# Performance work log

Hardware: AMD Instinct MI355X
Metric: run time of the kernel (lower is better)

Reference implementation:

```python
import jax, jax.numpy as jnp
import numpy as np

HIDDEN = 512
NUM_HEADS = 8
HEAD = HIDDEN // NUM_HEADS
TOP_K = 64
NEG = -1e9


def setup_inputs() -> dict:
    key = jax.random.key(0)
    ks = jax.random.split(key, 12)
    B, Q, S = 2, 2048, 4096
    sc = 0.02
    return {
        "main_input": jax.random.normal(ks[0], (B, Q, HIDDEN), jnp.float32),
        "side_input": jax.random.normal(ks[1], (S, HIDDEN), jnp.float32),
        "att_mask": jax.random.randint(ks[2], (B, Q, S), 0, 2, jnp.int32),
        "Wq": jax.random.normal(ks[3], (HIDDEN, HIDDEN), jnp.float32) * sc,
        "bq": jnp.zeros((HIDDEN,), jnp.float32),
        "Wk": jax.random.normal(ks[4], (HIDDEN, HIDDEN), jnp.float32) * sc,
        "bk": jnp.zeros((HIDDEN,), jnp.float32),
        "Wv": jax.random.normal(ks[5], (HIDDEN, HIDDEN), jnp.float32) * sc,
        "bv": jnp.zeros((HIDDEN,), jnp.float32),
        "Wo": jax.random.normal(ks[6], (HIDDEN, HIDDEN), jnp.float32) * sc,
        "bo": jnp.zeros((HIDDEN,), jnp.float32),
    }


def reference(main_input, side_input, att_mask, Wq, bq, Wk, bk, Wv, bv, Wo, bo):
    B, Qlen, _ = main_input.shape
    S = side_input.shape[0]
    # multi-head projections; side K/V shared across the whole batch
    q = (main_input @ Wq + bq).reshape(B, Qlen, NUM_HEADS, HEAD)
    k = (side_input @ Wk + bk).reshape(S, NUM_HEADS, HEAD)
    v = (side_input @ Wv + bv).reshape(S, NUM_HEADS, HEAD)
    # scores: [B, H, Q, S]
    scores = jnp.einsum("bqhd,khd->bhqk", q, k) / jnp.sqrt(jnp.asarray(HEAD, q.dtype))
    # attention mask (0 = masked)
    mask = att_mask[:, None, :, :].astype(scores.dtype)  # [B,1,Q,S]
    scores = scores + (1.0 - mask) * NEG
    # top-k restriction: keep only the TOP_K largest scores per query row
    thresh = jax.lax.top_k(scores, TOP_K)[0][..., -1:]  # kth largest
    scores = jnp.where(scores >= thresh, scores, NEG)
    probs = jax.nn.softmax(scores, axis=-1)
    ctx = jnp.einsum("bhqk,khd->bqhd", probs, v).reshape(B, Qlen, HIDDEN)
    return ctx @ Wo + bo
```

## Files before the change

### kernel.cpp

```cpp
#include <hip/hip_runtime.h>
#include <stdint.h>

typedef uint32_t u32;
typedef unsigned long long u64;

#define NEGV (-1e9f)
#define MAXSEL 128
#define NCAND 12

__device__ __forceinline__ u32 f2ord(float f) {
  u32 x = __float_as_uint(f);
  return (x & 0x80000000u) ? ~x : (x | 0x80000000u);
}
__device__ __forceinline__ float ord2f(u32 u) {
  u32 x = (u & 0x80000000u) ? (u ^ 0x80000000u) : ~u;
  return __uint_as_float(x);
}

__global__ __launch_bounds__(256)
void pack_mask(const int* __restrict__ mask, u64* __restrict__ mbits) {
  int w = blockIdx.x * 256 + threadIdx.x;
  const int4* p = (const int4*)(mask + (size_t)w * 64);
  u64 bits = 0;
#pragma unroll
  for (int j = 0; j < 16; ++j) {
    int4 m = p[j];
    if (m.x) bits |= 1ull << (j * 4 + 0);
    if (m.y) bits |= 1ull << (j * 4 + 1);
    if (m.z) bits |= 1ull << (j * 4 + 2);
    if (m.w) bits |= 1ull << (j * 4 + 3);
  }
  mbits[w] = bits;
}

__global__ __launch_bounds__(256)
void gemm_bias(const float* __restrict__ A, const float* __restrict__ W,
               const float* __restrict__ bias, float* __restrict__ C) {
  __shared__ float As[16][68];
  __shared__ float Bs[16][64];
  const int tid = threadIdx.x;
  const int tx = tid & 15, ty = tid >> 4;
  const int n0 = blockIdx.x << 6, m0 = blockIdx.y << 6;
  float c[4][4] = {};
  for (int k0 = 0; k0 < 512; k0 += 16) {
    {
      const int row = tid >> 2, kp = (tid & 3) << 2;
      float4 av = *(const float4*)&A[(size_t)(m0 + row) * 512 + k0 + kp];
      As[kp + 0][row] = av.x;
      As[kp + 1][row] = av.y;
      As[kp + 2][row] = av.z;
      As[kp + 3][row] = av.w;
      const int kk = tid >> 4, np = (tid & 15) << 2;
      *(float4*)&Bs[kk][np] = *(const float4*)&W[(size_t)(k0 + kk) * 512 + n0 + np];
    }
    __syncthreads();
#pragma unroll
    for (int kk = 0; kk < 16; ++kk) {
      float4 a = *(const float4*)&As[kk][ty << 2];
      float4 b = *(const float4*)&Bs[kk][tx << 2];
      c[0][0] += a.x * b.x; c[0][1] += a.x * b.y; c[0][2] += a.x * b.z; c[0][3] += a.x * b.w;
      c[1][0] += a.y * b.x; c[1][1] += a.y * b.y; c[1][2] += a.y * b.z; c[1][3] += a.y * b.w;
      c[2][0] += a.z * b.x; c[2][1] += a.z * b.y; c[2][2] += a.z * b.z; c[2][3] += a.z * b.w;
      c[3][0] += a.w * b.x; c[3][1] += a.w * b.y; c[3][2] += a.w * b.z; c[3][3] += a.w * b.w;
    }
    __syncthreads();
  }
  float4 bv = *(const float4*)&bias[n0 + (tx << 2)];
#pragma unroll
  for (int i = 0; i < 4; ++i) {
    float4 o;
    o.x = c[i][0] + bv.x; o.y = c[i][1] + bv.y;
    o.z = c[i][2] + bv.z; o.w = c[i][3] + bv.w;
    *(float4*)&C[(size_t)(m0 + (ty << 2) + i) * 512 + n0 + (tx << 2)] = o;
  }
}

__global__ __launch_bounds__(256)
void gemm_bias_T(const float* __restrict__ A, const float* __restrict__ W,
                 const float* __restrict__ bias, float* __restrict__ CT, int qsh) {
  __shared__ float As[16][68];
  __shared__ float Bs[16][64];
  const int tid = threadIdx.x;
  const int tx = tid & 15, ty = tid >> 4;
  const int n0 = blockIdx.x << 6, m0 = blockIdx.y << 6;
  float c[4][4] = {};
  for (int k0 = 0; k0 < 512; k0 += 16) {
    {
      const int row = tid >> 2, kp = (tid & 3) << 2;
      float4 av = *(const float4*)&A[(size_t)(m0 + row) * 512 + k0 + kp];
      As[kp + 0][row] = av.x;
      As[kp + 1][row] = av.y;
      As[kp + 2][row] = av.z;
      As[kp + 3][row] = av.w;
      const int kk = tid >> 4, np = (tid & 15) << 2;
      *(float4*)&Bs[kk][np] = *(const float4*)&W[(size_t)(k0 + kk) * 512 + n0 + np];
    }
    __syncthreads();
#pragma unroll
    for (int kk = 0; kk < 16; ++kk) {
      float4 a = *(const float4*)&As[kk][ty << 2];
      float4 b = *(const float4*)&Bs[kk][tx << 2];
      c[0][0] += a.x * b.x; c[0][1] += a.x * b.y; c[0][2] += a.x * b.z; c[0][3] += a.x * b.w;
      c[1][0] += a.y * b.x; c[1][1] += a.y * b.y; c[1][2] += a.y * b.z; c[1][3] += a.y * b.w;
      c[2][0] += a.z * b.x; c[2][1] += a.z * b.y; c[2][2] += a.z * b.z; c[2][3] += a.z * b.w;
      c[3][0] += a.w * b.x; c[3][1] += a.w * b.y; c[3][2] += a.w * b.z; c[3][3] += a.w * b.w;
    }
    __syncthreads();
  }
  float4 bv = *(const float4*)&bias[n0 + (tx << 2)];
  float bvv[4] = {bv.x, bv.y, bv.z, bv.w};
  const int qlen = 1 << qsh;
  const int qmask = qlen - 1;
#pragma unroll
  for (int i = 0; i < 4; ++i) {
#pragma unroll
    for (int j = 0; j < 4; ++j) {
      float val = c[i][j] + bvv[j];
      int m = m0 + (ty << 2) + i;
      int n = n0 + (tx << 2) + j;
      int h = n >> 6, d = n & 63;
      int bb = m >> qsh, q = m & qmask;
      CT[(((size_t)bb * 8 + h) * 64 + d) * qlen + q] = val;
    }
  }
}

__global__ __launch_bounds__(256)
void score_kernel(const float* __restrict__ qT, const float* __restrict__ kT,
                  const u64* __restrict__ mbits, float* __restrict__ sbuf, int sl0) {
  __shared__ float Qs[64][128];
  __shared__ float Ks[64][128];
  const int sl = sl0 + blockIdx.z;
  const int b = sl >> 3, h = sl & 7;
  const int s0 = blockIdx.x << 7, q0 = blockIdx.y << 7;
  const int tid = threadIdx.x;
  const float* qbase = qT + (size_t)sl * 64 * 2048 + q0;
  const float* kbase = kT + (size_t)h * 64 * 4096 + s0;
  float4* Qf = (float4*)&Qs[0][0];
  float4* Kf = (float4*)&Ks[0][0];
#pragma unroll
  for (int u = 0; u < 8; ++u) {
    int i = (u << 8) + tid;
    int row = i >> 5, col = (i & 31) << 2;
    Qf[i] = *(const float4*)(qbase + (size_t)row * 2048 + col);
    Kf[i] = *(const float4*)(kbase + (size_t)row * 4096 + col);
  }
  __syncthreads();
  const int tx = tid & 15, ty = tid >> 4;
  float c[8][8] = {};
#pragma unroll 4
  for (int g = 0; g < 16; ++g) {
    const int kk = g << 2;
    float qa[8][4], kb[8][4];
#pragma unroll
    for (int t = 0; t < 4; ++t) {
#pragma unroll
      for (int i = 0; i < 8; ++i) qa[i][t] = Qs[kk + t][(ty << 3) + i];
#pragma unroll
      for (int j = 0; j < 4; ++j) {
        kb[j][t]     = Ks[kk + t][(tx << 2) + j];
        kb[4 + j][t] = Ks[kk + t][64 + (tx << 2) + j];
      }
    }
#pragma unroll
    for (int i = 0; i < 8; ++i)
#pragma unroll
      for (int j = 0; j < 8; ++j)
        c[i][j] += qa[i][0] * kb[j][0] + qa[i][1] * kb[j][1]
                 + qa[i][2] * kb[j][2] + qa[i][3] * kb[j][3];
  }
  float* srow = sbuf + ((size_t)blockIdx.z * 2048 + q0) * 4096 + s0;
  const u64* mrow = mbits + ((size_t)(b * 2048 + q0)) * 64 + (s0 >> 6);
#pragma unroll
  for (int i = 0; i < 8; ++i) {
    const int row = (ty << 3) + i;
    u64 wA = mrow[(size_t)row * 64];
    u64 wB = mrow[(size_t)row * 64 + 1];
    float4 o0, o1;
    o0.x = ((wA >> ((tx << 2) + 0)) & 1) ? c[i][0] * 0.125f : NEGV;
    o0.y = ((wA >> ((tx << 2) + 1)) & 1) ? c[i][1] * 0.125f : NEGV;
    o0.z = ((wA >> ((tx << 2) + 2)) & 1) ? c[i][2] * 0.125f : NEGV;
    o0.w = ((wA >> ((tx << 2) + 3)) & 1) ? c[i][3] * 0.125f : NEGV;
    o1.x = ((wB >> ((tx << 2) + 0)) & 1) ? c[i][4] * 0.125f : NEGV;
    o1.y = ((wB >> ((tx << 2) + 1)) & 1) ? c[i][5] * 0.125f : NEGV;
    o1.z = ((wB >> ((tx << 2) + 2)) & 1) ? c[i][6] * 0.125f : NEGV;
    o1.w = ((wB >> ((tx << 2) + 3)) & 1) ? c[i][7] * 0.125f : NEGV;
    *(float4*)&srow[(size_t)row * 4096 + (tx << 2)] = o0;
    *(float4*)&srow[(size_t)row * 4096 + 64 + (tx << 2)] = o1;
  }
}

__global__ __launch_bounds__(256)
void select_kernel(const float* __restrict__ sbuf, const float* __restrict__ vbuf,
                   float* __restrict__ ctxbuf, int sl0) {
  const int sl = sl0 + blockIdx.y;
  const int b = sl >> 3, h = sl & 7;
  const int w = threadIdx.x >> 6, lane = threadIdx.x & 63;
  const int qi = (blockIdx.x << 2) + w;
  __shared__ u32  cv_lds[4][NCAND][64];
  __shared__ int  ci_lds[4][NCAND][64];
  __shared__ int   s_idx[4][MAXSEL];
  __shared__ float s_e[4][MAXSEL];

  const float* srow = sbuf + ((size_t)blockIdx.y * 2048 + qi) * 4096;
  const u32 ordneg = f2ord(NEGV);
  const u64 lmask_lt = (1ull << lane) - 1ull;

  u32 u[64];
#pragma unroll
  for (int j = 0; j < 16; ++j) {
    float4 v = *(const float4*)(srow + (j << 8) + (lane << 2));
    u[j * 4 + 0] = f2ord(v.x);
    u[j * 4 + 1] = f2ord(v.y);
    u[j * 4 + 2] = f2ord(v.z);
    u[j * 4 + 3] = f2ord(v.w);
  }
  u32 lmax = 0;
#pragma unroll
  for (int e = 0; e < 64; ++e) lmax = u[e] > lmax ? u[e] : lmax;
  u32 mx = lmax, mn = lmax;
#pragma unroll
  for (int off = 32; off; off >>= 1) {
    u32 a = (u32)__shfl_xor((int)mx, off, 64);
    u32 bq = (u32)__shfl_xor((int)mn, off, 64);
    mx = a > mx ? a : mx;
    mn = bq < mn ? bq : mn;
  }
  const float fm = ord2f(mx);
  const u32 lo0 = mn;

  int cnt = 0;
#pragma unroll
  for (int e = 0; e < 64; ++e) {
    u32 ue = u[e];
    if (ue >= lo0 && ue != ordneg) {
      if (cnt < NCAND) {
        cv_lds[w][cnt][lane] = ue;
        ci_lds[w][cnt][lane] = ((e >> 2) << 8) + (lane << 2) + (e & 3);
      }
      cnt++;
    }
  }
  const bool fallback = (__ballot(cnt > NCAND) != 0ull);

  u32 thr;
  int nsel;
  float esum = 0.f;

  if (!fallback) {
    asm volatile("s_waitcnt lgkmcnt(0)" ::: "memory");
    u32 cv[NCAND];
    int ci[NCAND];
#pragma unroll
    for (int j = 0; j < NCAND; ++j) {
      u32 raw = cv_lds[w][j][lane];
      cv[j] = (j < cnt) ? raw : 0u;
      ci[j] = ci_lds[w][j][lane];
    }
    u32 lo = lo0, hi = mx + 1;
    while (hi - lo > 1) {
      u32 mid = lo + ((hi - lo) >> 1);
      int c2 = 0;
#pragma unroll
      for (int j = 0; j < NCAND; ++j)
        c2 += __popcll(__ballot(cv[j] >= mid));
      if (c2 >= 64) lo = mid; else hi = mid;
    }
    thr = lo;
    int base = 0;
#pragma unroll
    for (int j = 0; j < NCAND; ++j) {
      bool pred = (j < cnt) && (cv[j] >= thr);
      u64 m = __ballot(pred);
      int ofs = base + __popcll(m & lmask_lt);
      if (pred && ofs < MAXSEL) {
        float ev = __expf(ord2f(cv[j]) - fm);
        s_idx[w][ofs] = ci[j];
        s_e[w][ofs] = ev;
        esum += ev;
      }
      base += (int)__popcll(m);
    }
    nsel = base < MAXSEL ? base : MAXSEL;
  } else {
    u32 lo = ordneg, hi = mx + 1;
    while (hi - lo > 1) {
      u32 mid = lo + ((hi - lo) >> 1);
      int c2 = 0;
#pragma unroll
      for (int e = 0; e < 64; ++e)
        c2 += __popcll(__ballot(u[e] >= mid));
      if (c2 >= 64) lo = mid; else hi = mid;
    }
    thr = lo;
    int base = 0;
#pragma unroll
    for (int e = 0; e < 64; ++e) {
      bool pred = (u[e] >= thr) && (u[e] != ordneg);
      u64 m = __ballot(pred);
      int ofs = base + __popcll(m & lmask_lt);
      if (pred && ofs < MAXSEL) {
        float ev = __expf(ord2f(u[e]) - fm);
        s_idx[w][ofs] = ((e >> 2) << 8) + (lane << 2) + (e & 3);
        s_e[w][ofs] = ev;
        esum += ev;
      }
      base += (int)__popcll(m);
    }
    nsel = base < MAXSEL ? base : MAXSEL;
  }

#pragma unroll
  for (int off = 32; off; off >>= 1) esum += __shfl_xor(esum, off, 64);
  const float rs = 1.0f / esum;
  asm volatile("s_waitcnt lgkmcnt(0)" ::: "memory");

  float acc = 0.f;
  const float* vb = vbuf + h * 64 + lane;
#pragma unroll 4
  for (int j = 0; j < nsel; ++j)
    acc += s_e[w][j] * vb[(size_t)s_idx[w][j] << 9];
  ctxbuf[((size_t)(b * 2048 + qi)) * 512 + h * 64 + lane] = acc * rs;
}

extern "C" void kernel_launch(void* const* d_in, const int* in_sizes, int n_in,
                              void* d_out, int out_size, void* d_ws, size_t ws_size,
                              hipStream_t stream) {
  const float* main_in = (const float*)d_in[0];
  const float* side_in = (const float*)d_in[1];
  const int*   mask    = (const int*)d_in[2];
  const float* Wq = (const float*)d_in[3];
  const float* bq = (const float*)d_in[4];
  const float* Wk = (const float*)d_in[5];
  const float* bk = (const float*)d_in[6];
  const float* Wv = (const float*)d_in[7];
  const float* bv = (const float*)d_in[8];
  const float* Wo = (const float*)d_in[9];
  const float* bo = (const float*)d_in[10];
  float* out = (float*)d_out;

  char* ws = (char*)d_ws;
  float* qT   = (float*)(ws);
  float* kT   = (float*)(ws + ((size_t)8 << 20));
  float* vbuf = (float*)(ws + ((size_t)16 << 20));
  float* ctxb = (float*)(ws + ((size_t)24 << 20));
  u64* mbits  = (u64*)(ws + ((size_t)32 << 20));
  float* sbuf = (float*)(ws + ((size_t)34 << 20));
  const size_t base = (size_t)34 << 20;
  const size_t sliceb = (size_t)2048 * 4096 * 4;

  int nz = 1;
  if (ws_size > base + sliceb) {
    size_t m = (ws_size - base) / sliceb;
    nz = (int)(m > 16 ? 16 : m);
  }

  pack_mask<<<1024, 256, 0, stream>>>(mask, mbits);
  gemm_bias_T<<<dim3(8, 64), 256, 0, stream>>>(main_in, Wq, bq, qT, 11);
  gemm_bias_T<<<dim3(8, 64), 256, 0, stream>>>(side_in, Wk, bk, kT, 12);
  gemm_bias  <<<dim3(8, 64), 256, 0, stream>>>(side_in, Wv, bv, vbuf);

  for (int sl0 = 0; sl0 < 16; sl0 += nz) {
    int z = nz < (16 - sl0) ? nz : (16 - sl0);
    score_kernel <<<dim3(32, 16, z), 256, 0, stream>>>(qT, kT, mbits, sbuf, sl0);
    select_kernel<<<dim3(512, z), 256, 0, stream>>>(sbuf, vbuf, ctxb, sl0);
  }

  gemm_bias<<<dim3(8, 64), 256, 0, stream>>>(ctxb, Wo, bo, out);
}
```

Measured before the change: 824.6 us.

## Restructure top-k select kernel to one wave per block with unified selection pass

The select kernel now runs one 64-lane wave per block (2048 blocks instead of 512 blocks of four waves), with launch bounds of (64, 2). The candidate count rises from 12 to 16. The index LDS array is dropped: after the threshold search, a single shared pass over all 64 register values builds a packed (index, exp) list in shared memory. The gather over V is unrolled into four independent accumulators over a list padded to a multiple of four, which increases memory-level parallelism. In exchange, every lane computes exp for all 64 elements, and the launch-bounds hint may change register allocation.

```diff
diff --git a/kernel.cpp b/kernel.cpp
--- a/kernel.cpp
+++ b/kernel.cpp
@@ -6,7 +6,7 @@
 
 #define NEGV (-1e9f)
 #define MAXSEL 128
-#define NCAND 12
+#define NCAND 16
 
 __device__ __forceinline__ u32 f2ord(float f) {
   u32 x = __float_as_uint(f);
@@ -190,17 +190,15 @@
   }
 }
 
-__global__ __launch_bounds__(256)
+__global__ __launch_bounds__(64, 2)
 void select_kernel(const float* __restrict__ sbuf, const float* __restrict__ vbuf,
                    float* __restrict__ ctxbuf, int sl0) {
   const int sl = sl0 + blockIdx.y;
   const int b = sl >> 3, h = sl & 7;
-  const int w = threadIdx.x >> 6, lane = threadIdx.x & 63;
-  const int qi = (blockIdx.x << 2) + w;
-  __shared__ u32  cv_lds[4][NCAND][64];
-  __shared__ int  ci_lds[4][NCAND][64];
-  __shared__ int   s_idx[4][MAXSEL];
-  __shared__ float s_e[4][MAXSEL];
+  const int qi = blockIdx.x;
+  const int lane = threadIdx.x;
+  __shared__ u32 cv_lds[NCAND][64];
+  __shared__ u64 list[MAXSEL];
 
   const float* srow = sbuf + ((size_t)blockIdx.y * 2048 + qi) * 4096;
   const u32 ordneg = f2ord(NEGV);
@@ -222,9 +220,9 @@
 #pragma unroll
   for (int off = 32; off; off >>= 1) {
     u32 a = (u32)__shfl_xor((int)mx, off, 64);
-    u32 bq = (u32)__shfl_xor((int)mn, off, 64);
+    u32 c = (u32)__shfl_xor((int)mn, off, 64);
     mx = a > mx ? a : mx;
-    mn = bq < mn ? bq : mn;
+    mn = c < mn ? c : mn;
   }
   const float fm = ord2f(mx);
   const u32 lo0 = mn;
@@ -234,30 +232,20 @@
   for (int e = 0; e < 64; ++e) {
     u32 ue = u[e];
     if (ue >= lo0 && ue != ordneg) {
-      if (cnt < NCAND) {
-        cv_lds[w][cnt][lane] = ue;
-        ci_lds[w][cnt][lane] = ((e >> 2) << 8) + (lane << 2) + (e & 3);
-      }
+      if (cnt < NCAND) cv_lds[cnt][lane] = ue;
       cnt++;
     }
   }
-  const bool fallback = (__ballot(cnt > NCAND) != 0ull);
-
-  u32 thr;
-  int nsel;
-  float esum = 0.f;
-
-  if (!fallback) {
-    asm volatile("s_waitcnt lgkmcnt(0)" ::: "memory");
+  const bool fb = (__ballot(cnt > NCAND) != 0ull);
+
+  u32 lo = lo0, hi = mx + 1;
+  if (!fb) {
+#pragma unroll
+    for (int j = 0; j < NCAND; ++j)
+      if (j >= cnt) cv_lds[j][lane] = 0;
     u32 cv[NCAND];
-    int ci[NCAND];
-#pragma unroll
-    for (int j = 0; j < NCAND; ++j) {
-      u32 raw = cv_lds[w][j][lane];
-      cv[j] = (j < cnt) ? raw : 0u;
-      ci[j] = ci_lds[w][j][lane];
-    }
-    u32 lo = lo0, hi = mx + 1;
+#pragma unroll
+    for (int j = 0; j < NCAND; ++j) cv[j] = cv_lds[j][lane];
     while (hi - lo > 1) {
       u32 mid = lo + ((hi - lo) >> 1);
       int c2 = 0;
@@ -266,24 +254,7 @@
         c2 += __popcll(__ballot(cv[j] >= mid));
       if (c2 >= 64) lo = mid; else hi = mid;
     }
-    thr = lo;
-    int base = 0;
-#pragma unroll
-    for (int j = 0; j < NCAND; ++j) {
-      bool pred = (j < cnt) && (cv[j] >= thr);
-      u64 m = __ballot(pred);
-      int ofs = base + __popcll(m & lmask_lt);
-      if (pred && ofs < MAXSEL) {
-        float ev = __expf(ord2f(cv[j]) - fm);
-        s_idx[w][ofs] = ci[j];
-        s_e[w][ofs] = ev;
-        esum += ev;
-      }
-      base += (int)__popcll(m);
-    }
-    nsel = base < MAXSEL ? base : MAXSEL;
   } else {
-    u32 lo = ordneg, hi = mx + 1;
     while (hi - lo > 1) {
       u32 mid = lo + ((hi - lo) >> 1);
       int c2 = 0;
@@ -292,34 +263,45 @@
         c2 += __popcll(__ballot(u[e] >= mid));
       if (c2 >= 64) lo = mid; else hi = mid;
     }
-    thr = lo;
-    int base = 0;
-#pragma unroll
-    for (int e = 0; e < 64; ++e) {
-      bool pred = (u[e] >= thr) && (u[e] != ordneg);
-      u64 m = __ballot(pred);
-      int ofs = base + __popcll(m & lmask_lt);
-      if (pred && ofs < MAXSEL) {
-        float ev = __expf(ord2f(u[e]) - fm);
-        s_idx[w][ofs] = ((e >> 2) << 8) + (lane << 2) + (e & 3);
-        s_e[w][ofs] = ev;
-        esum += ev;
-      }
-      base += (int)__popcll(m);
-    }
-    nsel = base < MAXSEL ? base : MAXSEL;
-  }
+  }
+  const u32 thr = lo;
+
+  float esum = 0.f;
+  int base = 0;
+#pragma unroll
+  for (int e = 0; e < 64; ++e) {
+    u32 ue = u[e];
+    bool pred = (ue >= thr) && (ue != ordneg);
+    float ev = __expf(ord2f(ue) - fm);
+    u64 m = __ballot(pred);
+    int ofs = base + __popcll(m & lmask_lt);
+    if (pred && ofs < MAXSEL) {
+      int sidx = ((e >> 2) << 8) + (lane << 2) + (e & 3);
+      list[ofs] = ((u64)(u32)sidx << 32) | (u64)__float_as_uint(ev);
+      esum += ev;
+    }
+    base += (int)__popcll(m);
+  }
+  int nsel = base < MAXSEL ? base : MAXSEL;
+  int pad = (4 - (nsel & 3)) & 3;
+  if (lane < pad && nsel + lane < MAXSEL) list[nsel + lane] = 0;
+  int n4 = nsel + pad;
+  if (n4 > MAXSEL) n4 = MAXSEL;
 
 #pragma unroll
   for (int off = 32; off; off >>= 1) esum += __shfl_xor(esum, off, 64);
   const float rs = 1.0f / esum;
-  asm volatile("s_waitcnt lgkmcnt(0)" ::: "memory");
-
-  float acc = 0.f;
+
   const float* vb = vbuf + h * 64 + lane;
-#pragma unroll 4
-  for (int j = 0; j < nsel; ++j)
-    acc += s_e[w][j] * vb[(size_t)s_idx[w][j] << 9];
+  float a0 = 0.f, a1 = 0.f, a2 = 0.f, a3 = 0.f;
+  for (int g = 0; g < n4; g += 4) {
+    u64 p0 = list[g + 0], p1 = list[g + 1], p2 = list[g + 2], p3 = list[g + 3];
+    a0 += __uint_as_float((u32)p0) * vb[(size_t)(p0 >> 32) * 512];
+    a1 += __uint_as_float((u32)p1) * vb[(size_t)(p1 >> 32) * 512];
+    a2 += __uint_as_float((u32)p2) * vb[(size_t)(p2 >> 32) * 512];
+    a3 += __uint_as_float((u32)p3) * vb[(size_t)(p3 >> 32) * 512];
+  }
+  float acc = (a0 + a1) + (a2 + a3);
   ctxbuf[((size_t)(b * 2048 + qi)) * 512 + h * 64 + lane] = acc * rs;
 }
 
@@ -363,7 +345,7 @@
   for (int sl0 = 0; sl0 < 16; sl0 += nz) {
     int z = nz < (16 - sl0) ? nz : (16 - sl0);
     score_kernel <<<dim3(32, 16, z), 256, 0, stream>>>(qT, kT, mbits, sbuf, sl0);
-    select_kernel<<<dim3(512, z), 256, 0, stream>>>(sbuf, vbuf, ctxb, sl0);
+    select_kernel<<<dim3(2048, z), 64, 0, stream>>>(sbuf, vbuf, ctxb, sl0);
   }
 
   gemm_bias<<<dim3(8, 64), 256, 0, stream>>>(ctxb, Wo, bo, out);
```

Result: slower. 860.7 us (+4.4%).
